# Kernel optimization log

Hardware: AMD Instinct MI355X
Metric: run time of the kernel (lower is better)

## Reference

```python
import jax, jax.numpy as jnp
import numpy as np
from jax import lax

B, T, H, C, D = 256, 512, 512, 10, 1


def _xavier(key, shape):
    fan_in, fan_out = shape[1], shape[0]
    lim = float(np.sqrt(6.0 / (fan_in + fan_out)))
    return jax.random.uniform(key, shape, jnp.float32, -lim, lim)


def setup_inputs() -> dict:
    key = jax.random.key(0)
    ks = jax.random.split(key, 10)
    return {
        "x": jax.random.normal(ks[0], (B, T), jnp.float32),
        "wgx": _xavier(ks[1], (H, D)), "wgh": _xavier(ks[2], (H, H)), "bg": jnp.zeros((H,), jnp.float32),
        "wix": _xavier(ks[3], (H, D)), "wih": _xavier(ks[4], (H, H)), "bi": jnp.zeros((H,), jnp.float32),
        "wfx": _xavier(ks[5], (H, D)), "wfh": _xavier(ks[6], (H, H)), "bf": 2.0 * jnp.ones((H,), jnp.float32),
        "wox": _xavier(ks[7], (H, D)), "woh": _xavier(ks[8], (H, H)), "bo": jnp.zeros((H,), jnp.float32),
        "wph": _xavier(ks[9], (C, H)), "bp": jnp.zeros((C,), jnp.float32),
    }


def reference(x, wgx, wgh, bg, wix, wih, bi, wfx, wfh, bf, wox, woh, bo, wph, bp):
    batch = x.shape[0]
    nh = wgh.shape[0]
    h0 = jnp.zeros((batch, nh), x.dtype)
    c0 = jnp.zeros((batch, nh), x.dtype)

    def step(carry, xt):
        h, c = carry
        xt = xt[:, None]  # [B, 1] scalar input per timestep
        # Faithful to source: x uses W.T, h uses W untransposed; g has no tanh.
        g = xt @ wgx.T + h @ wgh + bg
        i = jax.nn.sigmoid(xt @ wix.T + h @ wih + bi)
        f = jax.nn.sigmoid(xt @ wfx.T + h @ wfh + bf)
        o = jax.nn.sigmoid(xt @ wox.T + h @ woh + bo)
        c = g * i + c * f
        h = c * o  # no tanh on cell, as in source
        return (h, c), None

    (h, _), _ = lax.scan(step, (h0, c0), x.T)  # scan over time axis
    return h @ wph.T + bp
```

## Files before the change

### kernel.cpp

```cpp
#include <hip/hip_runtime.h>

#define B_   256
#define T_   512
#define H_   512
#define C_   10
#define NGRP 8
#define BPG  32
#define JT   16
#define NJT  32
#define KPAD 516
#define NTHR 256
#define LDS_BYTES (4 * JT * KPAD * 4)

__device__ __forceinline__ float expf_cephes(float x) {
    x = fminf(x, 88.3762626647949f);
    x = fmaxf(x, -88.3762626647949f);
    float fx = __fmaf_rn(x, 1.44269504088896341f, 0.5f);
    fx = floorf(fx);
    x = __fmaf_rn(fx, -0.693359375f, x);
    x = __fmaf_rn(fx, 2.12194440e-4f, x);
    float z = __fmul_rn(x, x);
    float y = 1.9875691500E-4f;
    y = __fmaf_rn(y, x, 1.3981999507E-3f);
    y = __fmaf_rn(y, x, 8.3334519073E-3f);
    y = __fmaf_rn(y, x, 4.1665795894E-2f);
    y = __fmaf_rn(y, x, 1.6666665459E-1f);
    y = __fmaf_rn(y, x, 5.0000001201E-1f);
    y = __fmaf_rn(y, z, x);
    y = __fadd_rn(y, 1.0f);
    return ldexpf(y, (int)fx);
}

__device__ __forceinline__ float sig_np(float pre) {
    float e = expf_cephes(-pre);
    return __fdiv_rn(1.0f, __fadd_rn(1.0f, e));
}

#define FMA8(h0, h1, w0, w1, w2, w3)                                          \
    a00 = __fmaf_rn((h0).x, (w0).x, a00); a00 = __fmaf_rn((h0).y, (w0).y, a00); \
    a00 = __fmaf_rn((h0).z, (w0).z, a00); a00 = __fmaf_rn((h0).w, (w0).w, a00); \
    a01 = __fmaf_rn((h0).x, (w1).x, a01); a01 = __fmaf_rn((h0).y, (w1).y, a01); \
    a01 = __fmaf_rn((h0).z, (w1).z, a01); a01 = __fmaf_rn((h0).w, (w1).w, a01); \
    a02 = __fmaf_rn((h0).x, (w2).x, a02); a02 = __fmaf_rn((h0).y, (w2).y, a02); \
    a02 = __fmaf_rn((h0).z, (w2).z, a02); a02 = __fmaf_rn((h0).w, (w2).w, a02); \
    a03 = __fmaf_rn((h0).x, (w3).x, a03); a03 = __fmaf_rn((h0).y, (w3).y, a03); \
    a03 = __fmaf_rn((h0).z, (w3).z, a03); a03 = __fmaf_rn((h0).w, (w3).w, a03); \
    a10 = __fmaf_rn((h1).x, (w0).x, a10); a10 = __fmaf_rn((h1).y, (w0).y, a10); \
    a10 = __fmaf_rn((h1).z, (w0).z, a10); a10 = __fmaf_rn((h1).w, (w0).w, a10); \
    a11 = __fmaf_rn((h1).x, (w1).x, a11); a11 = __fmaf_rn((h1).y, (w1).y, a11); \
    a11 = __fmaf_rn((h1).z, (w1).z, a11); a11 = __fmaf_rn((h1).w, (w1).w, a11); \
    a12 = __fmaf_rn((h1).x, (w2).x, a12); a12 = __fmaf_rn((h1).y, (w2).y, a12); \
    a12 = __fmaf_rn((h1).z, (w2).z, a12); a12 = __fmaf_rn((h1).w, (w2).w, a12); \
    a13 = __fmaf_rn((h1).x, (w3).x, a13); a13 = __fmaf_rn((h1).y, (w3).y, a13); \
    a13 = __fmaf_rn((h1).z, (w3).z, a13); a13 = __fmaf_rn((h1).w, (w3).w, a13);

#define LOADS(j, n)                                                           \
    hA##j = hr0[n]; hB##j = hr1[n];                                           \
    wG##j = wr0[n]; wI##j = wr1[n]; wF##j = wr2[n]; wO##j = wr3[n];

#define STEPF(j) FMA8(hA##j, hB##j, wG##j, wI##j, wF##j, wO##j)

__global__ void __launch_bounds__(NTHR, 1) lstm_fast(
    const float* __restrict__ x,
    const float* __restrict__ wgh, const float* __restrict__ wih,
    const float* __restrict__ wfh, const float* __restrict__ woh,
    const float* __restrict__ wgx, const float* __restrict__ wix,
    const float* __restrict__ wfx, const float* __restrict__ wox,
    const float* __restrict__ bgp, const float* __restrict__ bip,
    const float* __restrict__ bfp, const float* __restrict__ bop,
    float* __restrict__ hbuf, unsigned int* __restrict__ cnt)
{
    extern __shared__ float lds[];
    const int tid = threadIdx.x;
    const int bg  = blockIdx.x & (NGRP - 1);
    const int jt  = blockIdx.x >> 3;
    const int j0  = jt * JT;

    const float* wh[4] = {wgh, wih, wfh, woh};
    for (int g = 0; g < 4; ++g) {
        const float* w = wh[g];
        for (int idx = tid; idx < H_ * JT; idx += NTHR) {
            int k  = idx >> 4;
            int jj = idx & (JT - 1);
            lds[(g * JT + jj) * KPAD + k] = w[k * H_ + j0 + jj];
        }
    }
    __syncthreads();

    const int jl = tid & (JT - 1);
    const int b2 = tid >> 4;
    const int b0 = bg * BPG + b2 * 2;
    const int b1 = b0 + 1;
    const int jg = j0 + jl;

    const float wx0 = wgx[jg], wx1 = wix[jg], wx2 = wfx[jg], wx3 = wox[jg];
    const float bs0 = bgp[jg], bs1 = bip[jg], bs2 = bfp[jg], bs3 = bop[jg];

    const float4* wr0 = (const float4*)&lds[(0 * JT + jl) * KPAD];
    const float4* wr1 = (const float4*)&lds[(1 * JT + jl) * KPAD];
    const float4* wr2 = (const float4*)&lds[(2 * JT + jl) * KPAD];
    const float4* wr3 = (const float4*)&lds[(3 * JT + jl) * KPAD];

    float c0 = 0.f, c1 = 0.f;

    for (int t = 0; t < T_; ++t) {
        if (t > 0) {
            if (tid == 0) {
                while (__hip_atomic_load(&cnt[t * NGRP + bg], __ATOMIC_RELAXED,
                                         __HIP_MEMORY_SCOPE_AGENT) < NJT) {
                    __builtin_amdgcn_s_sleep(1);
                }
                (void)__hip_atomic_load(&cnt[t * NGRP + bg], __ATOMIC_ACQUIRE,
                                        __HIP_MEMORY_SCOPE_AGENT);
            }
            __syncthreads();
        }

        const float xt0 = x[b0 * T_ + t];
        const float xt1 = x[b1 * T_ + t];

        const float* hb = hbuf + (size_t)(t & 1) * B_ * H_;
        const float4* hr0 = (const float4*)(hb + b0 * H_);
        const float4* hr1 = (const float4*)(hb + b1 * H_);

        float a00 = 0.f, a01 = 0.f, a02 = 0.f, a03 = 0.f;
        float a10 = 0.f, a11 = 0.f, a12 = 0.f, a13 = 0.f;

        float4 hA0, hB0, wG0, wI0, wF0, wO0;
        float4 hA1, hB1, wG1, wI1, wF1, wO1;
        float4 hA2, hB2, wG2, wI2, wF2, wO2;
        float4 hA3, hB3, wG3, wI3, wF3, wO3;

        LOADS(0, 0) LOADS(1, 1) LOADS(2, 2) LOADS(3, 3)

        #pragma unroll 1
        for (int m = 0; m < 31; ++m) {
            const int n = 4 * m;
            STEPF(0) LOADS(0, n + 4)
            STEPF(1) LOADS(1, n + 5)
            STEPF(2) LOADS(2, n + 6)
            STEPF(3) LOADS(3, n + 7)
        }
        STEPF(0) STEPF(1) STEPF(2) STEPF(3)

        const float pg0 = __fadd_rn(__fadd_rn(__fmul_rn(wx0, xt0), a00), bs0);
        const float pi0 = __fadd_rn(__fadd_rn(__fmul_rn(wx1, xt0), a01), bs1);
        const float pf0 = __fadd_rn(__fadd_rn(__fmul_rn(wx2, xt0), a02), bs2);
        const float po0 = __fadd_rn(__fadd_rn(__fmul_rn(wx3, xt0), a03), bs3);
        const float i0 = sig_np(pi0), f0 = sig_np(pf0), o0 = sig_np(po0);
        c0 = __fadd_rn(__fmul_rn(pg0, i0), __fmul_rn(c0, f0));
        const float hn0 = __fmul_rn(c0, o0);

        const float pg1 = __fadd_rn(__fadd_rn(__fmul_rn(wx0, xt1), a10), bs0);
        const float pi1 = __fadd_rn(__fadd_rn(__fmul_rn(wx1, xt1), a11), bs1);
        const float pf1 = __fadd_rn(__fadd_rn(__fmul_rn(wx2, xt1), a12), bs2);
        const float po1 = __fadd_rn(__fadd_rn(__fmul_rn(wx3, xt1), a13), bs3);
        const float i1 = sig_np(pi1), f1 = sig_np(pf1), o1 = sig_np(po1);
        c1 = __fadd_rn(__fmul_rn(pg1, i1), __fmul_rn(c1, f1));
        const float hn1 = __fmul_rn(c1, o1);

        float* hw = hbuf + (size_t)((t + 1) & 1) * B_ * H_;
        hw[b0 * H_ + jg] = hn0;
        hw[b1 * H_ + jg] = hn1;

        __syncthreads();
        if (tid == 0) {
            __hip_atomic_fetch_add(&cnt[(t + 1) * NGRP + bg], 1u,
                                   __ATOMIC_RELEASE, __HIP_MEMORY_SCOPE_AGENT);
        }
    }
}

__global__ void __launch_bounds__(64) proj_kernel(
    const float* __restrict__ hbuf, const float* __restrict__ wph,
    const float* __restrict__ bp, float* __restrict__ out)
{
    const int b = blockIdx.x, tid = threadIdx.x;
    const float* h = hbuf + (size_t)b * H_;
    if (tid < C_) {
        float acc = 0.f;
        for (int k = 0; k < H_; ++k)
            acc = __fmaf_rn(h[k], wph[tid * H_ + k], acc);
        out[b * C_ + tid] = __fadd_rn(acc, bp[tid]);
    }
}

extern "C" void kernel_launch(void* const* d_in, const int* in_sizes, int n_in,
                              void* d_out, int out_size, void* d_ws, size_t ws_size,
                              hipStream_t stream)
{
    const float* x   = (const float*)d_in[0];
    const float* wgx = (const float*)d_in[1];
    const float* wgh = (const float*)d_in[2];
    const float* bgp = (const float*)d_in[3];
    const float* wix = (const float*)d_in[4];
    const float* wih = (const float*)d_in[5];
    const float* bip = (const float*)d_in[6];
    const float* wfx = (const float*)d_in[7];
    const float* wfh = (const float*)d_in[8];
    const float* bfp = (const float*)d_in[9];
    const float* wox = (const float*)d_in[10];
    const float* woh = (const float*)d_in[11];
    const float* bop = (const float*)d_in[12];
    const float* wph = (const float*)d_in[13];
    const float* bp  = (const float*)d_in[14];
    float* out = (float*)d_out;

    float* hbuf = (float*)d_ws;
    unsigned int* cnt = (unsigned int*)((char*)d_ws + (size_t)2 * B_ * H_ * 4);
    size_t zero_bytes = (size_t)2 * B_ * H_ * 4 + (size_t)(T_ + 1) * NGRP * 4;
    hipMemsetAsync(d_ws, 0, zero_bytes, stream);

    hipFuncSetAttribute((const void*)lstm_fast,
                        hipFuncAttributeMaxDynamicSharedMemorySize, LDS_BYTES);

    void* args[] = {&x, &wgh, &wih, &wfh, &woh, &wgx, &wix, &wfx, &wox,
                    &bgp, &bip, &bfp, &bop, &hbuf, &cnt};
    hipLaunchCooperativeKernel((const void*)lstm_fast, dim3(NGRP * NJT), dim3(NTHR),
                               args, LDS_BYTES, stream);

    proj_kernel<<<B_, 64, 0, stream>>>(hbuf, wph, bp, out);
}
```

Baseline: 9.779 ms.

## Remap threads to one gate column each over 8 batch rows with bpermute gate exchange

Changes the per-thread work split so that each lane owns one (gate, column) pair and accumulates 8 batch rows, instead of all 4 gates for 2 rows. Weights move to an interleaved LDS layout, so each wave reads one contiguous float4 per k-chunk, and the h rows are wave-uniform broadcast loads. Gate pre-activations are exchanged across lanes with ds_bpermute before the cell update. Every lane now evaluates the sigmoids redundantly and only the owning lanes store, which raises register pressure and adds cross-lane traffic in the epilogue.

```diff
diff --git a/kernel.cpp b/kernel.cpp
--- a/kernel.cpp
+++ b/kernel.cpp
@@ -8,9 +8,8 @@
 #define BPG  32
 #define JT   16
 #define NJT  32
-#define KPAD 516
 #define NTHR 256
-#define LDS_BYTES (4 * JT * KPAD * 4)
+#define LDS_BYTES (4 * JT * H_ * 4)
 
 __device__ __forceinline__ float expf_cephes(float x) {
     x = fminf(x, 88.3762626647949f);
@@ -36,29 +35,35 @@
     return __fdiv_rn(1.0f, __fadd_rn(1.0f, e));
 }
 
-#define FMA8(h0, h1, w0, w1, w2, w3)                                          \
-    a00 = __fmaf_rn((h0).x, (w0).x, a00); a00 = __fmaf_rn((h0).y, (w0).y, a00); \
-    a00 = __fmaf_rn((h0).z, (w0).z, a00); a00 = __fmaf_rn((h0).w, (w0).w, a00); \
-    a01 = __fmaf_rn((h0).x, (w1).x, a01); a01 = __fmaf_rn((h0).y, (w1).y, a01); \
-    a01 = __fmaf_rn((h0).z, (w1).z, a01); a01 = __fmaf_rn((h0).w, (w1).w, a01); \
-    a02 = __fmaf_rn((h0).x, (w2).x, a02); a02 = __fmaf_rn((h0).y, (w2).y, a02); \
-    a02 = __fmaf_rn((h0).z, (w2).z, a02); a02 = __fmaf_rn((h0).w, (w2).w, a02); \
-    a03 = __fmaf_rn((h0).x, (w3).x, a03); a03 = __fmaf_rn((h0).y, (w3).y, a03); \
-    a03 = __fmaf_rn((h0).z, (w3).z, a03); a03 = __fmaf_rn((h0).w, (w3).w, a03); \
-    a10 = __fmaf_rn((h1).x, (w0).x, a10); a10 = __fmaf_rn((h1).y, (w0).y, a10); \
-    a10 = __fmaf_rn((h1).z, (w0).z, a10); a10 = __fmaf_rn((h1).w, (w0).w, a10); \
-    a11 = __fmaf_rn((h1).x, (w1).x, a11); a11 = __fmaf_rn((h1).y, (w1).y, a11); \
-    a11 = __fmaf_rn((h1).z, (w1).z, a11); a11 = __fmaf_rn((h1).w, (w1).w, a11); \
-    a12 = __fmaf_rn((h1).x, (w2).x, a12); a12 = __fmaf_rn((h1).y, (w2).y, a12); \
-    a12 = __fmaf_rn((h1).z, (w2).z, a12); a12 = __fmaf_rn((h1).w, (w2).w, a12); \
-    a13 = __fmaf_rn((h1).x, (w3).x, a13); a13 = __fmaf_rn((h1).y, (w3).y, a13); \
-    a13 = __fmaf_rn((h1).z, (w3).z, a13); a13 = __fmaf_rn((h1).w, (w3).w, a13);
-
-#define LOADS(j, n)                                                           \
-    hA##j = hr0[n]; hB##j = hr1[n];                                           \
-    wG##j = wr0[n]; wI##j = wr1[n]; wF##j = wr2[n]; wO##j = wr3[n];
-
-#define STEPF(j) FMA8(hA##j, hB##j, wG##j, wI##j, wF##j, wO##j)
+#define FMA4(acc, h4, w4)                                                       \
+    acc = __fmaf_rn((h4).x, (w4).x, acc); acc = __fmaf_rn((h4).y, (w4).y, acc); \
+    acc = __fmaf_rn((h4).z, (w4).z, acc); acc = __fmaf_rn((h4).w, (w4).w, acc);
+
+#define STEPF(s)                                                                \
+    FMA4(a0, Ha##s, W##s) FMA4(a1, Hb##s, W##s) FMA4(a2, Hc##s, W##s)           \
+    FMA4(a3, Hd##s, W##s) FMA4(a4, He##s, W##s) FMA4(a5, Hf##s, W##s)           \
+    FMA4(a6, Hg##s, W##s) FMA4(a7, Hh##s, W##s)
+
+#define LOADS(s, n)                                                             \
+    W##s  = wr[((n) << 6) + l];                                                 \
+    Ha##s = hr0[n]; Hb##s = hr1[n]; Hc##s = hr2[n]; Hd##s = hr3[n];             \
+    He##s = hr4[n]; Hf##s = hr5[n]; Hg##s = hr6[n]; Hh##s = hr7[n];
+
+#define EPI(bi, av, cv)                                                         \
+    {                                                                           \
+        const float pre = __fadd_rn(__fadd_rn(__fmul_rn(wx, xt##bi), av), bs);  \
+        const int pbits = __float_as_int(pre);                                  \
+        const float pg = __int_as_float(__builtin_amdgcn_ds_bpermute(ix0, pbits)); \
+        const float pi = __int_as_float(__builtin_amdgcn_ds_bpermute(ix1, pbits)); \
+        const float pf = __int_as_float(__builtin_amdgcn_ds_bpermute(ix2, pbits)); \
+        const float po = __int_as_float(__builtin_amdgcn_ds_bpermute(ix3, pbits)); \
+        const float iv = sig_np(pi);                                            \
+        const float fv = sig_np(pf);                                            \
+        const float ov = sig_np(po);                                            \
+        cv = __fadd_rn(__fmul_rn(pg, iv), __fmul_rn(cv, fv));                   \
+        const float hn = __fmul_rn(cv, ov);                                     \
+        if (((bi) >> 1) == g) hwp[(bi) * H_] = hn;                              \
+    }
 
 __global__ void __launch_bounds__(NTHR, 1) lstm_fast(
     const float* __restrict__ x,
@@ -77,31 +82,38 @@
     const int j0  = jt * JT;
 
     const float* wh[4] = {wgh, wih, wfh, woh};
-    for (int g = 0; g < 4; ++g) {
-        const float* w = wh[g];
+    for (int g2 = 0; g2 < 4; ++g2) {
+        const float* w = wh[g2];
         for (int idx = tid; idx < H_ * JT; idx += NTHR) {
-            int k  = idx >> 4;
-            int jj = idx & (JT - 1);
-            lds[(g * JT + jj) * KPAD + k] = w[k * H_ + j0 + jj];
+            const int k   = idx >> 4;
+            const int jj2 = idx & (JT - 1);
+            lds[((k >> 2) << 8) + (((g2 << 4) + jj2) << 2) + (k & 3)] =
+                w[k * H_ + j0 + jj2];
         }
     }
     __syncthreads();
 
-    const int jl = tid & (JT - 1);
-    const int b2 = tid >> 4;
-    const int b0 = bg * BPG + b2 * 2;
-    const int b1 = b0 + 1;
-    const int jg = j0 + jl;
-
-    const float wx0 = wgx[jg], wx1 = wix[jg], wx2 = wfx[jg], wx3 = wox[jg];
-    const float bs0 = bgp[jg], bs1 = bip[jg], bs2 = bfp[jg], bs3 = bop[jg];
-
-    const float4* wr0 = (const float4*)&lds[(0 * JT + jl) * KPAD];
-    const float4* wr1 = (const float4*)&lds[(1 * JT + jl) * KPAD];
-    const float4* wr2 = (const float4*)&lds[(2 * JT + jl) * KPAD];
-    const float4* wr3 = (const float4*)&lds[(3 * JT + jl) * KPAD];
-
-    float c0 = 0.f, c1 = 0.f;
+    const int l   = tid & 63;
+    const int wv  = tid >> 6;
+    const int g   = l >> 4;
+    const int jj  = l & 15;
+    const int jg  = j0 + jj;
+    const int b0w = bg * BPG + wv * 8;
+
+    const float* wxs = (g == 0) ? wgx : (g == 1) ? wix : (g == 2) ? wfx : wox;
+    const float* bss = (g == 0) ? bgp : (g == 1) ? bip : (g == 2) ? bfp : bop;
+    const float wx = wxs[jg];
+    const float bs = bss[jg];
+
+    const int ix0 = (jj + 0)  << 2;
+    const int ix1 = (jj + 16) << 2;
+    const int ix2 = (jj + 32) << 2;
+    const int ix3 = (jj + 48) << 2;
+
+    const float4* wr = (const float4*)lds;
+
+    float c0 = 0.f, c1 = 0.f, c2 = 0.f, c3 = 0.f;
+    float c4 = 0.f, c5 = 0.f, c6 = 0.f, c7 = 0.f;
 
     for (int t = 0; t < T_; ++t) {
         if (t > 0) {
@@ -116,20 +128,33 @@
             __syncthreads();
         }
 
-        const float xt0 = x[b0 * T_ + t];
-        const float xt1 = x[b1 * T_ + t];
+        const float xt0 = x[(b0w + 0) * T_ + t];
+        const float xt1 = x[(b0w + 1) * T_ + t];
+        const float xt2 = x[(b0w + 2) * T_ + t];
+        const float xt3 = x[(b0w + 3) * T_ + t];
+        const float xt4 = x[(b0w + 4) * T_ + t];
+        const float xt5 = x[(b0w + 5) * T_ + t];
+        const float xt6 = x[(b0w + 6) * T_ + t];
+        const float xt7 = x[(b0w + 7) * T_ + t];
 
         const float* hb = hbuf + (size_t)(t & 1) * B_ * H_;
-        const float4* hr0 = (const float4*)(hb + b0 * H_);
-        const float4* hr1 = (const float4*)(hb + b1 * H_);
-
-        float a00 = 0.f, a01 = 0.f, a02 = 0.f, a03 = 0.f;
-        float a10 = 0.f, a11 = 0.f, a12 = 0.f, a13 = 0.f;
-
-        float4 hA0, hB0, wG0, wI0, wF0, wO0;
-        float4 hA1, hB1, wG1, wI1, wF1, wO1;
-        float4 hA2, hB2, wG2, wI2, wF2, wO2;
-        float4 hA3, hB3, wG3, wI3, wF3, wO3;
+        const float4* hr0 = (const float4*)(hb + (b0w + 0) * H_);
+        const float4* hr1 = (const float4*)(hb + (b0w + 1) * H_);
+        const float4* hr2 = (const float4*)(hb + (b0w + 2) * H_);
+        const float4* hr3 = (const float4*)(hb + (b0w + 3) * H_);
+        const float4* hr4 = (const float4*)(hb + (b0w + 4) * H_);
+        const float4* hr5 = (const float4*)(hb + (b0w + 5) * H_);
+        const float4* hr6 = (const float4*)(hb + (b0w + 6) * H_);
+        const float4* hr7 = (const float4*)(hb + (b0w + 7) * H_);
+
+        float a0 = 0.f, a1 = 0.f, a2 = 0.f, a3 = 0.f;
+        float a4 = 0.f, a5 = 0.f, a6 = 0.f, a7 = 0.f;
+
+        float4 W0, W1, W2, W3;
+        float4 Ha0, Hb0, Hc0, Hd0, He0, Hf0, Hg0, Hh0;
+        float4 Ha1, Hb1, Hc1, Hd1, He1, Hf1, Hg1, Hh1;
+        float4 Ha2, Hb2, Hc2, Hd2, He2, Hf2, Hg2, Hh2;
+        float4 Ha3, Hb3, Hc3, Hd3, He3, Hf3, Hg3, Hh3;
 
         LOADS(0, 0) LOADS(1, 1) LOADS(2, 2) LOADS(3, 3)
 
@@ -143,25 +168,11 @@
         }
         STEPF(0) STEPF(1) STEPF(2) STEPF(3)
 
-        const float pg0 = __fadd_rn(__fadd_rn(__fmul_rn(wx0, xt0), a00), bs0);
-        const float pi0 = __fadd_rn(__fadd_rn(__fmul_rn(wx1, xt0), a01), bs1);
-        const float pf0 = __fadd_rn(__fadd_rn(__fmul_rn(wx2, xt0), a02), bs2);
-        const float po0 = __fadd_rn(__fadd_rn(__fmul_rn(wx3, xt0), a03), bs3);
-        const float i0 = sig_np(pi0), f0 = sig_np(pf0), o0 = sig_np(po0);
-        c0 = __fadd_rn(__fmul_rn(pg0, i0), __fmul_rn(c0, f0));
-        const float hn0 = __fmul_rn(c0, o0);
-
-        const float pg1 = __fadd_rn(__fadd_rn(__fmul_rn(wx0, xt1), a10), bs0);
-        const float pi1 = __fadd_rn(__fadd_rn(__fmul_rn(wx1, xt1), a11), bs1);
-        const float pf1 = __fadd_rn(__fadd_rn(__fmul_rn(wx2, xt1), a12), bs2);
-        const float po1 = __fadd_rn(__fadd_rn(__fmul_rn(wx3, xt1), a13), bs3);
-        const float i1 = sig_np(pi1), f1 = sig_np(pf1), o1 = sig_np(po1);
-        c1 = __fadd_rn(__fmul_rn(pg1, i1), __fmul_rn(c1, f1));
-        const float hn1 = __fmul_rn(c1, o1);
-
-        float* hw = hbuf + (size_t)((t + 1) & 1) * B_ * H_;
-        hw[b0 * H_ + jg] = hn0;
-        hw[b1 * H_ + jg] = hn1;
+        float* hw  = hbuf + (size_t)((t + 1) & 1) * B_ * H_;
+        float* hwp = hw + b0w * H_ + jg;
+
+        EPI(0, a0, c0) EPI(1, a1, c1) EPI(2, a2, c2) EPI(3, a3, c3)
+        EPI(4, a4, c4) EPI(5, a5, c5) EPI(6, a6, c6) EPI(7, a7, c7)
 
         __syncthreads();
         if (tid == 0) {
```

Result: slower. 22.75 ms (+132.6%).
